# Kernel optimization log

Measured on AMD Instinct MI355X. Metric: run time of the kernel, lower is better.

Reference implementation:

```python
import jax, jax.numpy as jnp
import numpy as np

N0, N1, N2, N3, B = 120000, 20000, 6000, 1600, 64
E1, E2, E3 = 480000, 144000, 38400
KS = 5  # kernel size per dim; K = 125 total


def spline_basis(pseudo, ks=KS):
    # open B-spline basis, degree 1, over [0,1]^3 (torch_spline_conv semantics)
    p = pseudo * (ks - 1)                       # (E,3)
    lo = jnp.clip(jnp.floor(p), 0.0, ks - 2.0)  # (E,3)
    f = p - lo                                  # fractional part
    bits = jnp.array([[(s >> d) & 1 for d in range(3)] for s in range(8)],
                     dtype=jnp.float32)         # (8,3) corner offsets
    w = jnp.where(bits[None] > 0, f[:, None, :], 1.0 - f[:, None, :])  # (E,8,3)
    basis = w[..., 0] * w[..., 1] * w[..., 2]   # (E,8)
    strides = jnp.array([1.0, ks, ks * ks], dtype=jnp.float32)
    kidx = ((lo[:, None, :] + bits[None]) * strides).sum(-1).astype(jnp.int32)  # (E,8)
    return basis, kidx


def spline_conv(x, edge_index, pseudo, W, root, bias, num_nodes):
    src, dst = edge_index[0], edge_index[1]
    basis, kidx = spline_basis(pseudo)                   # (E,8), (E,8)
    XW = jnp.einsum('ni,kio->nko', x, W)                 # (N,K,out)
    taps = XW[src[:, None], kidx]                        # (E,8,out) gather
    msg = (taps * basis[..., None]).sum(axis=1)          # (E,out)
    agg = jax.ops.segment_sum(msg, dst, num_segments=num_nodes)
    deg = jax.ops.segment_sum(jnp.ones_like(dst, jnp.float32), dst,
                              num_segments=num_nodes)
    agg = agg / jnp.maximum(deg, 1.0)[:, None]           # mean aggregation
    return agg + x @ root + bias


def seg_max(x, seg, n):
    v = jax.ops.segment_max(x, seg, num_segments=n)
    return jnp.where(jnp.isfinite(v), v, 0.0)  # empty voxels -> 0


def setup_inputs() -> dict:
    key = jax.random.key(0)
    ks = jax.random.split(key, 24)
    return {
        'x0': jax.random.uniform(ks[0], (N0, 1), jnp.float32),
        'cluster0': jax.random.randint(ks[1], (N0,), 0, N1),
        'edge1': jax.random.randint(ks[2], (2, E1), 0, N1),
        'pseudo1': jax.random.uniform(ks[3], (E1, 3), jnp.float32),
        'W1': jax.random.normal(ks[4], (125, 1, 64), jnp.float32) * 0.1,
        'root1': jax.random.normal(ks[5], (1, 64), jnp.float32) * 0.1,
        'b1': jnp.zeros((64,), jnp.float32),
        'cluster1': jax.random.randint(ks[6], (N1,), 0, N2),
        'edge2': jax.random.randint(ks[7], (2, E2), 0, N2),
        'pseudo2': jax.random.uniform(ks[8], (E2, 3), jnp.float32),
        'W2': jax.random.normal(ks[9], (125, 64, 64), jnp.float32) * 0.05,
        'root2': jax.random.normal(ks[10], (64, 64), jnp.float32) * 0.05,
        'b2': jnp.zeros((64,), jnp.float32),
        'cluster2': jax.random.randint(ks[11], (N2,), 0, N3),
        'edge3': jax.random.randint(ks[12], (2, E3), 0, N3),
        'pseudo3': jax.random.uniform(ks[13], (E3, 3), jnp.float32),
        'W3': jax.random.normal(ks[14], (125, 64, 128), jnp.float32) * 0.05,
        'root3': jax.random.normal(ks[15], (64, 128), jnp.float32) * 0.05,
        'b3': jnp.zeros((128,), jnp.float32),
        'cluster3': jax.random.randint(ks[16], (N3,), 0, B * 8),
        'fc1_w': jax.random.normal(ks[17], (1024, 256), jnp.float32) * 0.03,
        'fc1_b': jnp.zeros((256,), jnp.float32),
        'fc2_w': jax.random.normal(ks[18], (256, 10), jnp.float32) * 0.06,
        'fc2_b': jnp.zeros((10,), jnp.float32),
    }


def reference(x0, cluster0, edge1, pseudo1, W1, root1, b1,
              cluster1, edge2, pseudo2, W2, root2, b2,
              cluster2, edge3, pseudo3, W3, root3, b3,
              cluster3, fc1_w, fc1_b, fc2_w, fc2_b):
    x = seg_max(x0, cluster0, N1)                       # sparse voxel max pool 1
    x = jax.nn.elu(spline_conv(x, edge1, pseudo1, W1, root1, b1, N1))
    x = seg_max(x, cluster1, N2)                        # pool 2
    x = jax.nn.elu(spline_conv(x, edge2, pseudo2, W2, root2, b2, N2))
    x = seg_max(x, cluster2, N3)                        # pool 3
    x = jax.nn.elu(spline_conv(x, edge3, pseudo3, W3, root3, b3, N3))
    x = seg_max(x, cluster3, B * 8)                     # dense 2x2x2 voxel pool
    x = x.reshape(B, 8 * 128)
    x = jax.nn.elu(x @ fc1_w + fc1_b)
    x = x @ fc2_w + fc2_b
    return jax.nn.log_softmax(x, axis=1)
```

## Files before the change

### kernel.cpp

```cpp
#include <hip/hip_runtime.h>
#include <hip/hip_bf16.h>
#include <hip/hip_fp16.h>
#include <math.h>

#define N0c 120000
#define N1c 20000
#define N2c 6000
#define N3c 1600
#define E1c 480000
#define E2c 144000
#define E3c 38400

#define HB1 256
#define HB2 480
#define HB3 160
#define WCVB 125
#define SS0B  469

typedef __attribute__((ext_vector_type(8))) short short8;
typedef __attribute__((ext_vector_type(4))) float f32x4;

__device__ __forceinline__ float eluf(float x) {
    return x > 0.0f ? x : expm1f(x);
}

__device__ __forceinline__ unsigned f2sort(float f) {
    unsigned u = __float_as_uint(f);
    return (u & 0x80000000u) ? ~u : (u | 0x80000000u);
}
__device__ __forceinline__ float sort2f(unsigned u) {
    unsigned bits = (u & 0x80000000u) ? (u & 0x7FFFFFFFu) : ~u;
    return __uint_as_float(bits);
}
__device__ __forceinline__ unsigned short f2bf(float v) {
    unsigned u = __float_as_uint(v);
    unsigned r = (u + 0x7FFFu + ((u >> 16) & 1u)) >> 16;
    return (unsigned short)r;
}
__device__ __forceinline__ unsigned short f2h(float v) {
    return __half_as_ushort(__float2half(v));
}
__device__ __forceinline__ float h2f(unsigned short u) {
    return __half2float(__ushort_as_half(u));
}

__global__ __launch_bounds__(256) void hist_all(
    const int* __restrict__ edge1, const int* __restrict__ edge2,
    const int* __restrict__ edge3,
    const float* __restrict__ pseudo2, const float* __restrict__ pseudo3,
    const float* __restrict__ W2, const float* __restrict__ W3,
    const float* __restrict__ x0, const int* __restrict__ cluster0,
    int* __restrict__ cntD1,
    int* __restrict__ blockCnt2, int* __restrict__ binTot2, int* __restrict__ cntD2,
    int* __restrict__ blockCnt3, int* __restrict__ binTot3, int* __restrict__ cntD3,
    unsigned short* __restrict__ W2t, unsigned short* __restrict__ W3t,
    unsigned* __restrict__ xm1)
{
    __shared__ float smf[64 * 129];
    int* h = (int*)smf;
    int b = blockIdx.x, t = threadIdx.x;
    if (b < HB1) {
        for (int e = b * 256 + t; e < E1c; e += HB1 * 256)
            atomicAdd(&cntD1[edge1[E1c + e]], 1);
    } else if (b < HB1 + HB2 + HB3) {
        bool is2 = b < HB1 + HB2;
        int rb = is2 ? (b - HB1) : (b - HB1 - HB2);
        int nblk = is2 ? HB2 : HB3;
        int E = is2 ? E2c : E3c;
        const int* edge = is2 ? edge2 : edge3;
        const float* pseudo = is2 ? pseudo2 : pseudo3;
        int* blockCnt = is2 ? blockCnt2 : blockCnt3;
        int* binTot = is2 ? binTot2 : binTot3;
        int* dstCnt = is2 ? cntD2 : cntD3;
        int nb = is2 ? HB2 : HB3;
        if (t < 64) h[t] = 0;
        __syncthreads();
        for (int e = rb * 256 + t; e < E; e += nblk * 256) {
            int c = 0, mul = 1;
            #pragma unroll
            for (int d = 0; d < 3; d++) {
                float p = pseudo[e * 3 + d] * 4.0f;
                float l = fminf(fmaxf(floorf(p), 0.0f), 3.0f);
                c += (int)l * mul;
                mul <<= 2;
            }
            atomicAdd(&h[c], 1);
            atomicAdd(&dstCnt[edge[E + e]], 1);
        }
        __syncthreads();
        if (t < 64) {
            int v = h[t];
            blockCnt[t * nb + rb] = v;
            if (v) atomicAdd(&binTot[t], v);
        }
    } else if (b < HB1 + HB2 + HB3 + WCVB) {
        int k = b - (HB1 + HB2 + HB3);
        for (int idx = t; idx < 4096; idx += 256) {
            int n = idx & 63, ic = idx >> 6;
            smf[ic * 65 + n] = W2[((size_t)k * 64 + ic) * 64 + n];
        }
        __syncthreads();
        for (int idx = t; idx < 4096; idx += 256) {
            int ic = idx & 63, n = idx >> 6;
            W2t[((size_t)k * 64 + n) * 64 + ic] = f2bf(smf[ic * 65 + n]);
        }
    } else if (b < HB1 + HB2 + HB3 + 2 * WCVB) {
        int k = b - (HB1 + HB2 + HB3 + WCVB);
        for (int idx = t; idx < 8192; idx += 256) {
            int n = idx & 127, ic = idx >> 7;
            smf[ic * 129 + n] = W3[((size_t)k * 64 + ic) * 128 + n];
        }
        __syncthreads();
        for (int idx = t; idx < 8192; idx += 256) {
            int ic = idx & 63, n = idx >> 6;
            W3t[((size_t)k * 128 + n) * 64 + ic] = f2bf(smf[ic * 129 + n]);
        }
    } else {
        int idx = (b - (HB1 + HB2 + HB3 + 2 * WCVB)) * 256 + t;
        if (idx < N0c)
            atomicMax(&xm1[cluster0[idx]], f2sort(x0[idx]));
    }
}

__global__ __launch_bounds__(256) void plan_tot(
    const int* __restrict__ cntD1, int* __restrict__ dstStart1,
    const int* __restrict__ binTot2, int* __restrict__ binCnt2,
    int* __restrict__ binStart2, int* __restrict__ blkPrefix2,
    int* __restrict__ chunkBin2, int* __restrict__ chunkOff2,
    const int* __restrict__ binTot3, int* __restrict__ binCnt3,
    int* __restrict__ binStart3, int* __restrict__ blkPrefix3,
    int* __restrict__ chunkBin3, int* __restrict__ chunkOff3,
    const int* __restrict__ cntD2, int* __restrict__ dstStart2,
    const int* __restrict__ cntD3, int* __restrict__ dstStart3)
{
    __shared__ int ps[256];
    __shared__ int ps64[64];
    int t = threadIdx.x;

    {
        int4 locd[20];
        const int4* src = (const int4*)cntD1;
        #pragma unroll
        for (int i = 0; i < 20; i++) locd[i] = src[t * 20 + i];
        int sum = 0;
        #pragma unroll
        for (int i = 0; i < 20; i++)
            sum += locd[i].x + locd[i].y + locd[i].z + locd[i].w;
        ps[t] = sum;
        __syncthreads();
        for (int ofs = 1; ofs < 256; ofs <<= 1) {
            int add = (t >= ofs) ? ps[t - ofs] : 0;
            __syncthreads();
            ps[t] += add;
            __syncthreads();
        }
        int run = (t == 0) ? 0 : ps[t - 1];
        int base = t * 80;
        #pragma unroll
        for (int i = 0; i < 20; i++) {
            int b0 = base + i * 4;
            if (b0 < N1c) {
                dstStart1[b0] = run; run += locd[i].x;
                dstStart1[b0 + 1] = run; run += locd[i].y;
                dstStart1[b0 + 2] = run; run += locd[i].z;
                dstStart1[b0 + 3] = run; run += locd[i].w;
            }
        }
        if (t == 249) dstStart1[N1c] = run;
    }
    __syncthreads();

    if (t < 64) {
        int v = binTot2[t];
        binCnt2[t] = v;
        ps64[t] = v;
    }
    __syncthreads();
    if (t == 0) {
        int s2 = 0, p = 0;
        for (int c = 0; c < 64; c++) {
            int v = ps64[c];
            binStart2[c] = s2;
            blkPrefix2[c] = p;
            s2 += v;
            p += (v + 63) >> 6;
        }
        binStart2[64] = s2;
        blkPrefix2[64] = p;
    }
    __syncthreads();
    if (t < 64) {
        int nch = (binCnt2[t] + 63) >> 6;
        int base = blkPrefix2[t];
        for (int j = 0; j < nch; j++) {
            chunkBin2[base + j] = t;
            chunkOff2[base + j] = j;
        }
    }
    __syncthreads();

    if (t < 64) {
        int v = binTot3[t];
        binCnt3[t] = v;
        ps64[t] = v;
    }
    __syncthreads();
    if (t == 0) {
        int s3 = 0, p = 0;
        for (int c = 0; c < 64; c++) {
            int v = ps64[c];
            binStart3[c] = s3;
            blkPrefix3[c] = p;
            s3 += v;
            p += (v + 63) >> 6;
        }
        binStart3[64] = s3;
        blkPrefix3[64] = p;
    }
    __syncthreads();
    if (t < 64) {
        int nch = (binCnt3[t] + 63) >> 6;
        int base = blkPrefix3[t];
        for (int j = 0; j < nch; j++) {
            chunkBin3[base + j] = t;
            chunkOff3[base + j] = j;
        }
    }
    __syncthreads();

    {
        int locd[24];
        int sd = 0;
        #pragma unroll
        for (int i = 0; i < 24; i++) {
            int bin = t * 24 + i;
            int vv = (bin < N2c) ? cntD2[bin] : 0;
            locd[i] = vv;
            sd += vv;
        }
        ps[t] = sd;
        __syncthreads();
        for (int ofs = 1; ofs < 256; ofs <<= 1) {
            int add = (t >= ofs) ? ps[t - ofs] : 0;
            __syncthreads();
            ps[t] += add;
            __syncthreads();
        }
        int rund = (t == 0) ? 0 : ps[t - 1];
        #pragma unroll
        for (int i = 0; i < 24; i++) {
            int bin = t * 24 + i;
            if (bin < N2c) { dstStart2[bin] = rund; rund += locd[i]; }
        }
        if (t == 255) dstStart2[N2c] = ps[255];
    }
    __syncthreads();

    {
        int locd[7];
        int sd = 0;
        #pragma unroll
        for (int i = 0; i < 7; i++) {
            int bin = t * 7 + i;
            int vv = (bin < N3c) ? cntD3[bin] : 0;
            locd[i] = vv;
            sd += vv;
        }
        ps[t] = sd;
        __syncthreads();
        for (int ofs = 1; ofs < 256; ofs <<= 1) {
            int add = (t >= ofs) ? ps[t - ofs] : 0;
            __syncthreads();
            ps[t] += add;
            __syncthreads();
        }
        int rund = (t == 0) ? 0 : ps[t - 1];
        #pragma unroll
        for (int i = 0; i < 7; i++) {
            int bin = t * 7 + i;
            if (bin < N3c) { dstStart3[bin] = rund; rund += locd[i]; }
        }
        if (t == 255) dstStart3[N3c] = ps[255];
    }
}

__global__ __launch_bounds__(256) void off_all(
    const int* __restrict__ blockCnt2, const int* __restrict__ binStart2,
    int* __restrict__ blockOff2,
    const int* __restrict__ blockCnt3, const int* __restrict__ binStart3,
    int* __restrict__ blockOff3)
{
    int wid = (blockIdx.x * 256 + threadIdx.x) >> 6;
    int lane = threadIdx.x & 63;
    if (wid >= 128) return;
    const int* c;
    int* o;
    int run, width;
    if (wid < 64) {
        c = blockCnt2 + (size_t)wid * HB2;
        o = blockOff2 + (size_t)wid * HB2;
        run = binStart2[wid];
        width = HB2;
    } else {
        int bin = wid - 64;
        c = blockCnt3 + (size_t)bin * HB3;
        o = blockOff3 + (size_t)bin * HB3;
        run = binStart3[bin];
        width = HB3;
    }
    for (int base = 0; base < width; base += 64) {
        int b = base + lane;
        int v = (b < width) ? c[b] : 0;
        int inc = v;
        #pragma unroll
        for (int ofs = 1; ofs < 64; ofs <<= 1) {
            int u = __shfl_up(inc, ofs);
            if (lane >= ofs) inc += u;
        }
        if (b < width) o[b] = run + inc - v;
        run += __shfl(inc, 63);
    }
}

__global__ __launch_bounds__(256) void scatter_all(
    const int* __restrict__ edge1, const float* __restrict__ pseudo1,
    const int* __restrict__ edge2, const float* __restrict__ pseudo2,
    const int* __restrict__ edge3, const float* __restrict__ pseudo3,
    const int* __restrict__ dstStart1, int* __restrict__ curD1,
    const int* __restrict__ blockOff2, const int* __restrict__ blockOff3,
    int4* __restrict__ rec1, int4* __restrict__ rec2, int4* __restrict__ rec3,
    unsigned* __restrict__ xm1,
    const int* __restrict__ dstStart2, const int* __restrict__ dstStart3,
    int* __restrict__ curD2, int* __restrict__ curD3,
    int* __restrict__ posList2, int* __restrict__ posList3)
{
    __shared__ int cur[64];
    int b = blockIdx.x, t = threadIdx.x;
    if (b < HB1) {
        for (int e = b * 256 + t; e < E1c; e += HB1 * 256) {
            int src = edge1[e], dst = edge1[E1c + e];
            float f[3];
            int kbase = 0, mul5 = 1;
            #pragma unroll
            for (int d = 0; d < 3; d++) {
                float pp = pseudo1[e * 3 + d] * 4.0f;
                float l = fminf(fmaxf(floorf(pp), 0.0f), 3.0f);
                f[d] = pp - l;
                kbase += (int)l * mul5;
                mul5 *= 5;
            }
            int p = dstStart1[dst] + atomicAdd(&curD1[dst], 1);
            rec1[p] = make_int4(src | ((dst & 15) << 16) | (kbase << 20),
                                __float_as_int(f[0]), __float_as_int(f[1]),
                                __float_as_int(f[2]));
        }
    } else if (b < HB1 + HB2 + HB3) {
        bool is2 = b < HB1 + HB2;
        int rb = is2 ? (b - HB1) : (b - HB1 - HB2);
        int nblk = is2 ? HB2 : HB3;
        int E = is2 ? E2c : E3c;
        const int* edge = is2 ? edge2 : edge3;
        const float* pseudo = is2 ? pseudo2 : pseudo3;
        const int* blockOff = is2 ? blockOff2 : blockOff3;
        int4* rec = is2 ? rec2 : rec3;
        const int* dstStart = is2 ? dstStart2 : dstStart3;
        int* curD = is2 ? curD2 : curD3;
        int* posList = is2 ? posList2 : posList3;
        int nb = is2 ? HB2 : HB3;
        if (t < 64) cur[t] = blockOff[(size_t)t * nb + rb];
        __syncthreads();
        for (int e = rb * 256 + t; e < E; e += nblk * 256) {
            int src = edge[e], dst = edge[E + e];
            float f[3];
            int c = 0, mul = 1;
            #pragma unroll
            for (int d = 0; d < 3; d++) {
                float pp = pseudo[e * 3 + d] * 4.0f;
                float l = fminf(fmaxf(floorf(pp), 0.0f), 3.0f);
                f[d] = pp - l;
                c += (int)l * mul;
                mul <<= 2;
            }
            int p = atomicAdd(&cur[c], 1);
            rec[p] = make_int4(src | (dst << 16),
                               __float_as_int(f[0]), __float_as_int(f[1]),
                               __float_as_int(f[2]));
            int qd = dstStart[dst] + atomicAdd(&curD[dst], 1);
            posList[qd] = p;
        }
    } else {
        int idx = (b - (HB1 + HB2 + HB3)) * 256 + t;
        if (idx < N1c) {
            float f = sort2f(xm1[idx]);
            unsigned bb = __float_as_uint(f);
            if ((bb & 0x7F800000u) == 0x7F800000u) f = 0.0f;
            ((float*)xm1)[idx] = f;
        }
    }
}

__global__ __launch_bounds__(256) void conv1_block(
    const int4* __restrict__ rec, const float* __restrict__ x,
    const int* __restrict__ dstStart1,
    const float* __restrict__ W, const float* __restrict__ root,
    const float* __restrict__ bias, const int* __restrict__ cl,
    unsigned* __restrict__ xmOut) {
    __shared__ float T[16][128];
    int b = blockIdx.x;
    for (int j = threadIdx.x; j < 2048; j += 256) ((float*)T)[j] = 0.0f;
    __syncthreads();
    int v0 = b << 4;
    int s0 = dstStart1[v0], s1 = dstStart1[v0 + 16];
    for (int i = s0 + threadIdx.x; i < s1; i += 256) {
        int4 r = rec[i];
        int src = r.x & 0xFFFF;
        int ln = (r.x >> 16) & 15;
        int kbase = r.x >> 20;
        float f0 = __int_as_float(r.y);
        float f1 = __int_as_float(r.z);
        float f2 = __int_as_float(r.w);
        float xv = x[src];
        #pragma unroll
        for (int s = 0; s < 8; s++) {
            int b0 = s & 1, b1 = (s >> 1) & 1, b2 = (s >> 2) & 1;
            float w0 = b0 ? f0 : 1.0f - f0;
            float w1 = b1 ? f1 : 1.0f - f1;
            float w2 = b2 ? f2 : 1.0f - f2;
            int k = kbase + b0 + 5 * b1 + 25 * b2;
            atomicAdd(&T[ln][k], xv * w0 * w1 * w2);
        }
    }
    __syncthreads();
    int w = threadIdx.x >> 6, lane = threadIdx.x & 63;
    float acc[4] = {0.0f, 0.0f, 0.0f, 0.0f};
    for (int k = 0; k < 125; k++) {
        float wv = W[(k << 6) + lane];
        #pragma unroll
        for (int j = 0; j < 4; j++)
            acc[j] = fmaf(T[w + 4 * j][k], wv, acc[j]);
    }
    #pragma unroll
    for (int j = 0; j < 4; j++) {
        int ln = w + 4 * j;
        int v = v0 + ln;
        float d = fmaxf((float)(dstStart1[v + 1] - dstStart1[v]), 1.0f);
        float val = eluf(acc[j] / d + x[v] * root[lane] + bias[lane]);
        atomicMax(&xmOut[((size_t)cl[v] << 6) + lane], f2sort(val));
    }
}

__global__ void decode_cvt(unsigned* __restrict__ buf,
                           unsigned short* __restrict__ xb, int total) {
    int idx = blockIdx.x * blockDim.x + threadIdx.x;
    if (idx >= total) return;
    float f = sort2f(buf[idx]);
    unsigned b = __float_as_uint(f);
    if ((b & 0x7F800000u) == 0x7F800000u) f = 0.0f;
    ((float*)buf)[idx] = f;
    xb[idx] = f2bf(f);
}

template<int COUT>
__global__ __launch_bounds__(256) void spline_mfma(
    const int4* __restrict__ recs,
    const unsigned short* __restrict__ Wt,
    const unsigned short* __restrict__ xb,
    const int* __restrict__ binStart,
    const int* __restrict__ binCnt,
    const int* __restrict__ blkPrefix,
    const int* __restrict__ chunkBin,
    const int* __restrict__ chunkOff,
    unsigned short* __restrict__ msg)
{
    __shared__ float basisS[4][8][64];
    __shared__ int srcS[4][64];

    int w = threadIdx.x >> 6, lane = threadIdx.x & 63;
    int c = blockIdx.x * 4 + w;
    if (c >= blkPrefix[64]) return;
    int bin = chunkBin[c];
    int chunk = chunkOff[c];
    int cnt = binCnt[bin];

    {
        int pos = chunk * 64 + lane;
        bool act = pos < cnt;
        int4 r = act ? recs[binStart[bin] + pos] : make_int4(0, 0, 0, 0);
        srcS[w][lane] = r.x & 0xFFFF;
        float f0 = __int_as_float(r.y);
        float f1 = __int_as_float(r.z);
        float f2 = __int_as_float(r.w);
        #pragma unroll
        for (int s = 0; s < 8; s++) {
            float w0 = (s & 1) ? f0 : 1.0f - f0;
            float w1 = (s & 2) ? f1 : 1.0f - f1;
            float w2 = (s & 4) ? f2 : 1.0f - f2;
            basisS[w][s][lane] = act ? (w0 * w1 * w2) : 0.0f;
        }
    }
    __builtin_amdgcn_wave_barrier();
    __threadfence_block();

    int lo0 = bin & 3, lo1 = (bin >> 2) & 3, lo2 = bin >> 4;
    int kbase = lo0 + 5 * lo1 + 25 * lo2;
    int colOff = (COUT == 128) ? (blockIdx.y << 6) : 0;
    int q = lane >> 4;
    int mcol = lane & 15;

    short8 afr[4][2];
    #pragma unroll
    for (int rt = 0; rt < 4; rt++) {
        int src = srcS[w][rt * 16 + mcol];
        const unsigned short* xr = xb + ((size_t)src << 6) + q * 8;
        afr[rt][0] = *(const short8*)(xr);
        afr[rt][1] = *(const short8*)(xr + 32);
    }

    f32x4 acc[4][4];
    #pragma unroll
    for (int rt = 0; rt < 4; rt++)
        #pragma unroll
        for (int nt = 0; nt < 4; nt++)
            acc[rt][nt] = (f32x4){0.0f, 0.0f, 0.0f, 0.0f};
    const f32x4 zero4 = {0.0f, 0.0f, 0.0f, 0.0f};

    #pragma unroll 1
    for (int s = 0; s < 8; s++) {
        int k = kbase + (s & 1) + 5 * ((s >> 1) & 1) + 25 * (s >> 2);
        const unsigned short* Wk = Wt + ((size_t)k * COUT + colOff) * 64;
        short8 bfr[4][2];
        #pragma unroll
        for (int nt = 0; nt < 4; nt++) {
            const unsigned short* Wn = Wk + (size_t)(nt * 16 + mcol) * 64 + q * 8;
            bfr[nt][0] = *(const short8*)(Wn);
            bfr[nt][1] = *(const short8*)(Wn + 32);
        }
        #pragma unroll
        for (int rt = 0; rt < 4; rt++) {
            f32x4 ct[4];
            #pragma unroll
            for (int nt = 0; nt < 4; nt++) {
                ct[nt] = __builtin_amdgcn_mfma_f32_16x16x32_bf16(afr[rt][0], bfr[nt][0], zero4, 0, 0, 0);
                ct[nt] = __builtin_amdgcn_mfma_f32_16x16x32_bf16(afr[rt][1], bfr[nt][1], ct[nt], 0, 0, 0);
            }
            #pragma unroll
            for (int r = 0; r < 4; r++) {
                float bs = basisS[w][s][rt * 16 + q * 4 + r];
                #pragma unroll
                for (int nt = 0; nt < 4; nt++)
                    acc[rt][nt][r] = fmaf(bs, ct[nt][r], acc[rt][nt][r]);
            }
        }
    }

    int base = binStart[bin] + chunk * 64;
    #pragma unroll
    for (int rt = 0; rt < 4; rt++) {
        #pragma unroll
        for (int r = 0; r < 4; r++) {
            int row = rt * 16 + q * 4 + r;
            if (chunk * 64 + row < cnt) {
                unsigned short* mp = msg + (size_t)(base + row) * COUT + colOff + mcol;
                #pragma unroll
                for (int nt = 0; nt < 4; nt++)
                    mp[nt * 16] = f2h(acc[rt][nt][r]);
            }
        }
    }
}

__global__ __launch_bounds__(256) void agg_update64(
    const unsigned short* __restrict__ msg, const int* __restrict__ posList,
    const int* __restrict__ dstStart,
    const float* __restrict__ xm, const float* __restrict__ root,
    const float* __restrict__ bias, const int* __restrict__ cl,
    unsigned* __restrict__ xmOut, int nNodes) {
    __shared__ float xsh[4][64];
    int w = threadIdx.x >> 6, lane = threadIdx.x & 63;
    int v = blockIdx.x * 4 + w;
    if (v >= nNodes) return;
    xsh[w][lane] = xm[((size_t)v << 6) + lane];
    int s0 = dstStart[v], s1 = dstStart[v + 1];
    float a0 = 0.0f, a1 = 0.0f, a2 = 0.0f, a3 = 0.0f;
    int i = s0;
    for (; i + 4 <= s1; i += 4) {
        int p0 = posList[i], p1 = posList[i + 1];
        int p2 = posList[i + 2], p3 = posList[i + 3];
        a0 += h2f(msg[((size_t)p0 << 6) + lane]);
        a1 += h2f(msg[((size_t)p1 << 6) + lane]);
        a2 += h2f(msg[((size_t)p2 << 6) + lane]);
        a3 += h2f(msg[((size_t)p3 << 6) + lane]);
    }
    for (; i < s1; i++)
        a0 += h2f(msg[((size_t)posList[i] << 6) + lane]);
    float a = (a0 + a1 + a2 + a3) / fmaxf((float)(s1 - s0), 1.0f);
    float r = 0.0f;
    #pragma unroll 8
    for (int j = 0; j < 64; j++)
        r = fmaf(xsh[w][j], root[(j << 6) + lane], r);
    float val = eluf(a + r + bias[lane]);
    atomicMax(&xmOut[((size_t)cl[v] << 6) + lane], f2sort(val));
}

__global__ __launch_bounds__(256) void agg_update128(
    const unsigned short* __restrict__ msg, const int* __restrict__ posList,
    const int* __restrict__ dstStart,
    const float* __restrict__ xm, const float* __restrict__ root,
    const float* __restrict__ bias, const int* __restrict__ cl,
    unsigned* __restrict__ xmOut, int nNodes) {
    __shared__ float xsh[4][64];
    int w = threadIdx.x >> 6, lane = threadIdx.x & 63;
    int v = blockIdx.x * 4 + w;
    if (v >= nNodes) return;
    xsh[w][lane] = xm[((size_t)v << 6) + lane];
    int s0 = dstStart[v], s1 = dstStart[v + 1];
    float c0a = 0.0f, c0b = 0.0f, c1a = 0.0f, c1b = 0.0f;
    int i = s0;
    for (; i + 2 <= s1; i += 2) {
        int p0 = posList[i], p1 = posList[i + 1];
        const unsigned short* m0 = msg + ((size_t)p0 << 7);
        const unsigned short* m1 = msg + ((size_t)p1 << 7);
        c0a += h2f(m0[lane]); c0b += h2f(m0[64 + lane]);
        c1a += h2f(m1[lane]); c1b += h2f(m1[64 + lane]);
    }
    for (; i < s1; i++) {
        const unsigned short* m0 = msg + ((size_t)posList[i] << 7);
        c0a += h2f(m0[lane]); c0b += h2f(m0[64 + lane]);
    }
    float dinv = 1.0f / fmaxf((float)(s1 - s0), 1.0f);
    float aa0 = (c0a + c1a) * dinv;
    float aa1 = (c0b + c1b) * dinv;
    float r0 = 0.0f, r1 = 0.0f;
    #pragma unroll 8
    for (int j = 0; j < 64; j++) {
        float xi = xsh[w][j];
        r0 = fmaf(xi, root[(j << 7) + lane], r0);
        r1 = fmaf(xi, root[(j << 7) + 64 + lane], r1);
    }
    unsigned* orow = xmOut + ((size_t)cl[v] << 7);
    atomicMax(&orow[lane], f2sort(eluf(aa0 + r0 + bias[lane])));
    atomicMax(&orow[64 + lane], f2sort(eluf(aa1 + r1 + bias[lane + 64])));
}

__global__ __launch_bounds__(256) void fc1_split(
    const unsigned* __restrict__ xin, const float* __restrict__ w1,
    float* __restrict__ h) {
    __shared__ float xsh[128];
    int row = blockIdx.x, ks = blockIdx.y;
    int o = threadIdx.x;
    if (o < 128) {
        float f = sort2f(xin[row * 1024 + ks * 128 + o]);
        unsigned bb = __float_as_uint(f);
        if ((bb & 0x7F800000u) == 0x7F800000u) f = 0.0f;
        xsh[o] = f;
    }
    __syncthreads();
    float acc = 0.0f;
    const float* wp = w1 + (size_t)ks * 128 * 256 + o;
    #pragma unroll 8
    for (int i = 0; i < 128; i++)
        acc = fmaf(xsh[i], wp[i * 256], acc);
    atomicAdd(&h[row * 256 + o], acc);
}

__global__ __launch_bounds__(64) void fc2_k(
    const float* __restrict__ h, const float* __restrict__ b1,
    const float* __restrict__ w2, const float* __restrict__ b2,
    float* __restrict__ out) {
    __shared__ float hs[256];
    __shared__ float lg[10];
    int row = blockIdx.x;
    int t = threadIdx.x;
    for (int i = t; i < 256; i += 64) hs[i] = eluf(h[row * 256 + i] + b1[i]);
    __syncthreads();
    if (t < 10) {
        float a = b2[t];
        for (int i = 0; i < 256; i++) a = fmaf(hs[i], w2[i * 10 + t], a);
        lg[t] = a;
    }
    __syncthreads();
    if (t < 10) {
        float m = -1e30f;
        #pragma unroll
        for (int j = 0; j < 10; j++) m = fmaxf(m, lg[j]);
        float sum = 0.0f;
        #pragma unroll
        for (int j = 0; j < 10; j++) sum += expf(lg[j] - m);
        out[row * 10 + t] = lg[t] - m - logf(sum);
    }
}

extern "C" void kernel_launch(void* const* d_in, const int* in_sizes, int n_in,
                              void* d_out, int out_size, void* d_ws, size_t ws_size,
                              hipStream_t stream) {
    const float* x0      = (const float*)d_in[0];
    const int*   cluster0= (const int*)d_in[1];
    const int*   edge1   = (const int*)d_in[2];
    const float* pseudo1 = (const float*)d_in[3];
    const float* W1      = (const float*)d_in[4];
    const float* root1   = (const float*)d_in[5];
    const float* b1      = (const float*)d_in[6];
    const int*   cluster1= (const int*)d_in[7];
    const int*   edge2   = (const int*)d_in[8];
    const float* pseudo2 = (const float*)d_in[9];
    const float* W2      = (const float*)d_in[10];
    const float* root2   = (const float*)d_in[11];
    const float* b2      = (const float*)d_in[12];
    const int*   cluster2= (const int*)d_in[13];
    const int*   edge3   = (const int*)d_in[14];
    const float* pseudo3 = (const float*)d_in[15];
    const float* W3      = (const float*)d_in[16];
    const float* root3   = (const float*)d_in[17];
    const float* b3      = (const float*)d_in[18];
    const int*   cluster3= (const int*)d_in[19];
    const float* fc1_w   = (const float*)d_in[20];
    const float* fc1_b   = (const float*)d_in[21];
    const float* fc2_w   = (const float*)d_in[22];
    const float* fc2_b   = (const float*)d_in[23];
    float* out = (float*)d_out;

    float* ws = (float*)d_ws;
    size_t off = 0;
    float* xm1  = ws + off; off += 20480;
    float* xm2  = ws + off; off += (size_t)N2c * 64;
    float* xm3  = ws + off; off += (size_t)N3c * 64;
    float* xm4  = ws + off; off += 512 * 128;
    float* h1   = ws + off; off += 64 * 256;
    int* cntD1   = (int*)(ws + off); off += 20480;
    int* curD1   = (int*)(ws + off); off += 20032;
    int* cntD2   = (int*)(ws + off); off += 6016;
    int* cntD3   = (int*)(ws + off); off += 1664;
    int* curD2   = (int*)(ws + off); off += 6016;
    int* curD3   = (int*)(ws + off); off += 1664;
    int* binTot2 = (int*)(ws + off); off += 64;
    int* binTot3 = (int*)(ws + off); off += 64;
    size_t zeroFloats = off;
    int4* rec1 = (int4*)(ws + off); off += (size_t)E1c * 4;
    int4* rec2 = (int4*)(ws + off); off += (size_t)E2c * 4;
    int4* rec3 = (int4*)(ws + off); off += (size_t)E3c * 4;
    unsigned short* W2t = (unsigned short*)(ws + off); off += 256000;
    unsigned short* W3t = (unsigned short*)(ws + off); off += 512000;
    unsigned short* xb2 = (unsigned short*)(ws + off); off += 192000;
    unsigned short* xb3 = (unsigned short*)(ws + off); off += 51200;
    int* dstStart1 = (int*)(ws + off); off += 20032;
    int* blockCnt2 = (int*)(ws + off); off += (size_t)HB2 * 64;
    int* blockOff2 = (int*)(ws + off); off += (size_t)HB2 * 64;
    int* blockCnt3 = (int*)(ws + off); off += (size_t)HB3 * 64;
    int* blockOff3 = (int*)(ws + off); off += (size_t)HB3 * 64;
    int* binCnt2   = (int*)(ws + off); off += 64;
    int* binStart2 = (int*)(ws + off); off += 80;
    int* blkPrefix2= (int*)(ws + off); off += 80;
    int* chunkBin2 = (int*)(ws + off); off += 2560;
    int* chunkOff2 = (int*)(ws + off); off += 2560;
    int* binCnt3   = (int*)(ws + off); off += 64;
    int* binStart3 = (int*)(ws + off); off += 80;
    int* blkPrefix3= (int*)(ws + off); off += 80;
    int* chunkBin3 = (int*)(ws + off); off += 768;
    int* chunkOff3 = (int*)(ws + off); off += 768;
    int* dstStart2 = (int*)(ws + off); off += 6016;
    int* dstStart3 = (int*)(ws + off); off += 1664;
    int* posList2  = (int*)(ws + off); off += E2c;
    int* posList3  = (int*)(ws + off); off += E3c;
    unsigned short* msg = (unsigned short*)(ws + off); off += (size_t)E2c * 32;

    hipMemsetAsync(d_ws, 0, zeroFloats * sizeof(float), stream);

    hist_all<<<HB1 + HB2 + HB3 + 2 * WCVB + SS0B, 256, 0, stream>>>(
        edge1, edge2, edge3, pseudo2, pseudo3, W2, W3, x0, cluster0,
        cntD1, blockCnt2, binTot2, cntD2,
        blockCnt3, binTot3, cntD3, W2t, W3t, (unsigned*)xm1);

    plan_tot<<<1, 256, 0, stream>>>(
        cntD1, dstStart1,
        binTot2, binCnt2, binStart2, blkPrefix2, chunkBin2, chunkOff2,
        binTot3, binCnt3, binStart3, blkPrefix3, chunkBin3, chunkOff3,
        cntD2, dstStart2, cntD3, dstStart3);

    off_all<<<32, 256, 0, stream>>>(
        blockCnt2, binStart2, blockOff2,
        blockCnt3, binStart3, blockOff3);

    scatter_all<<<HB1 + HB2 + HB3 + (N1c + 255) / 256, 256, 0, stream>>>(
        edge1, pseudo1, edge2, pseudo2, edge3, pseudo3,
        dstStart1, curD1, blockOff2, blockOff3, rec1, rec2, rec3, (unsigned*)xm1,
        dstStart2, dstStart3, curD2, curD3, posList2, posList3);

    conv1_block<<<1250, 256, 0, stream>>>(rec1, xm1, dstStart1, W1, root1, b1,
                                          cluster1, (unsigned*)xm2);
    decode_cvt<<<(N2c * 64) / 256, 256, 0, stream>>>((unsigned*)xm2, xb2, N2c * 64);

    spline_mfma<64><<<dim3((E2c / 64 + 64 + 3) / 4, 1), 256, 0, stream>>>(
        rec2, W2t, xb2, binStart2, binCnt2, blkPrefix2, chunkBin2, chunkOff2, msg);
    agg_update64<<<(N2c + 3) / 4, 256, 0, stream>>>(msg, posList2, dstStart2,
                                                    xm2, root2, b2, cluster2,
                                                    (unsigned*)xm3, N2c);
    decode_cvt<<<(N3c * 64) / 256, 256, 0, stream>>>((unsigned*)xm3, xb3, N3c * 64);

    spline_mfma<128><<<dim3((E3c / 64 + 64 + 3) / 4, 2), 256, 0, stream>>>(
        rec3, W3t, xb3, binStart3, binCnt3, blkPrefix3, chunkBin3, chunkOff3, msg);
    agg_update128<<<(N3c + 3) / 4, 256, 0, stream>>>(msg, posList3, dstStart3,
                                                     xm3, root3, b3, cluster3,
                                                     (unsigned*)xm4, N3c);

    fc1_split<<<dim3(64, 8), 256, 0, stream>>>((unsigned*)xm4, fc1_w, h1);
    fc2_k<<<64, 64, 0, stream>>>(h1, fc1_b, fc2_w, fc2_b, out);
}
```

Baseline: 354.5 us.

## Compute conv1 per node with wavefront-per-node edge loop over LDS weights

Replaces the block-of-16-nodes conv1 kernel, which scattered basis-weighted inputs into a shared kernel-tap table with atomics and then did a 125-tap matmul, with a kernel that assigns one wavefront per destination node. Each lane owns one output channel and accumulates the 8 spline taps of every incoming edge directly against the weights staged in LDS. This removes the shared-memory atomics and the dense tap matmul, but every block now reloads the full 32KB weight table into LDS and runs four times as many blocks. The dst-lane bits are also dropped from the packed edge record.

```diff
diff --git a/kernel.cpp b/kernel.cpp
--- a/kernel.cpp
+++ b/kernel.cpp
@@ -350,7 +350,7 @@
                 mul5 *= 5;
             }
             int p = dstStart1[dst] + atomicAdd(&curD1[dst], 1);
-            rec1[p] = make_int4(src | ((dst & 15) << 16) | (kbase << 20),
+            rec1[p] = make_int4(src | (kbase << 20),
                                 __float_as_int(f[0]), __float_as_int(f[1]),
                                 __float_as_int(f[2]));
         }
@@ -399,54 +399,44 @@
     }
 }
 
-__global__ __launch_bounds__(256) void conv1_block(
+__global__ __launch_bounds__(256) void conv1_node(
     const int4* __restrict__ rec, const float* __restrict__ x,
     const int* __restrict__ dstStart1,
     const float* __restrict__ W, const float* __restrict__ root,
     const float* __restrict__ bias, const int* __restrict__ cl,
-    unsigned* __restrict__ xmOut) {
-    __shared__ float T[16][128];
-    int b = blockIdx.x;
-    for (int j = threadIdx.x; j < 2048; j += 256) ((float*)T)[j] = 0.0f;
-    __syncthreads();
-    int v0 = b << 4;
-    int s0 = dstStart1[v0], s1 = dstStart1[v0 + 16];
-    for (int i = s0 + threadIdx.x; i < s1; i += 256) {
+    unsigned* __restrict__ xmOut, int nNodes) {
+    __shared__ float Wl[125 * 64];
+    int t = threadIdx.x;
+    for (int i = t; i < 8000; i += 256) Wl[i] = W[i];
+    __syncthreads();
+    int w = t >> 6, lane = t & 63;
+    int v = blockIdx.x * 4 + w;
+    if (v >= nNodes) return;
+    int s0 = dstStart1[v], s1 = dstStart1[v + 1];
+    float acc = 0.0f;
+    #pragma unroll 2
+    for (int i = s0; i < s1; i++) {
         int4 r = rec[i];
         int src = r.x & 0xFFFF;
-        int ln = (r.x >> 16) & 15;
         int kbase = r.x >> 20;
         float f0 = __int_as_float(r.y);
         float f1 = __int_as_float(r.z);
         float f2 = __int_as_float(r.w);
         float xv = x[src];
-        #pragma unroll
-        for (int s = 0; s < 8; s++) {
-            int b0 = s & 1, b1 = (s >> 1) & 1, b2 = (s >> 2) & 1;
-            float w0 = b0 ? f0 : 1.0f - f0;
-            float w1 = b1 ? f1 : 1.0f - f1;
-            float w2 = b2 ? f2 : 1.0f - f2;
-            int k = kbase + b0 + 5 * b1 + 25 * b2;
-            atomicAdd(&T[ln][k], xv * w0 * w1 * w2);
-        }
-    }
-    __syncthreads();
-    int w = threadIdx.x >> 6, lane = threadIdx.x & 63;
-    float acc[4] = {0.0f, 0.0f, 0.0f, 0.0f};
-    for (int k = 0; k < 125; k++) {
-        float wv = W[(k << 6) + lane];
-        #pragma unroll
-        for (int j = 0; j < 4; j++)
-            acc[j] = fmaf(T[w + 4 * j][k], wv, acc[j]);
-    }
-    #pragma unroll
-    for (int j = 0; j < 4; j++) {
-        int ln = w + 4 * j;
-        int v = v0 + ln;
-        float d = fmaxf((float)(dstStart1[v + 1] - dstStart1[v]), 1.0f);
-        float val = eluf(acc[j] / d + x[v] * root[lane] + bias[lane]);
-        atomicMax(&xmOut[((size_t)cl[v] << 6) + lane], f2sort(val));
-    }
+        float g0 = 1.0f - f0, g1 = 1.0f - f1, g2 = 1.0f - f2;
+        const float* Wb = Wl + (kbase << 6) + lane;
+        acc = fmaf(xv * g0 * g1 * g2, Wb[0],       acc);
+        acc = fmaf(xv * f0 * g1 * g2, Wb[64],      acc);
+        acc = fmaf(xv * g0 * f1 * g2, Wb[5 * 64],  acc);
+        acc = fmaf(xv * f0 * f1 * g2, Wb[6 * 64],  acc);
+        acc = fmaf(xv * g0 * g1 * f2, Wb[25 * 64], acc);
+        acc = fmaf(xv * f0 * g1 * f2, Wb[26 * 64], acc);
+        acc = fmaf(xv * g0 * f1 * f2, Wb[30 * 64], acc);
+        acc = fmaf(xv * f0 * f1 * f2, Wb[31 * 64], acc);
+    }
+    float d = fmaxf((float)(s1 - s0), 1.0f);
+    float val = eluf(acc / d + x[v] * root[lane] + bias[lane]);
+    atomicMax(&xmOut[((size_t)cl[v] << 6) + lane], f2sort(val));
 }
 
 __global__ void decode_cvt(unsigned* __restrict__ buf,
@@ -785,8 +775,9 @@
         dstStart1, curD1, blockOff2, blockOff3, rec1, rec2, rec3, (unsigned*)xm1,
         dstStart2, dstStart3, curD2, curD3, posList2, posList3);
 
-    conv1_block<<<1250, 256, 0, stream>>>(rec1, xm1, dstStart1, W1, root1, b1,
-                                          cluster1, (unsigned*)xm2);
+    conv1_node<<<(N1c + 3) / 4, 256, 0, stream>>>(rec1, xm1, dstStart1, W1,
+                                                  root1, b1, cluster1,
+                                                  (unsigned*)xm2, N1c);
     decode_cvt<<<(N2c * 64) / 256, 256, 0, stream>>>((unsigned*)xm2, xb2, N2c * 64);
 
     spline_mfma<64><<<dim3((E2c / 64 + 64 + 3) / 4, 1), 256, 0, stream>>>(
```

After: 370.9 us. +4.6%, slower.
